# Kernel tuning notes

Measured on AMD Instinct MI355X. Metric: run time of the kernel, lower is better.

The kernel has to match this reference:

```python
import jax, jax.numpy as jnp
import numpy as np

N_NODES = 100000
N_EDGES = 1000000
F_IN = 256
HEADS = 2
C_OUT = 64
NEG_SLOPE = 0.2


def setup_inputs() -> dict:
    key = jax.random.key(0)
    k_x, k_e, k_ws, k_wd, k_a = jax.random.split(key, 5)
    x = jax.random.normal(k_x, (N_NODES, F_IN), dtype=jnp.float32)
    edge_index = jax.random.randint(k_e, (2, N_EDGES), 0, N_NODES, dtype=jnp.int64)
    # uniform init as in init_randoms('uniform'), scale is irrelevant for correctness
    W_src = jax.random.uniform(k_ws, (F_IN, HEADS * C_OUT), dtype=jnp.float32, minval=-0.1, maxval=0.1)
    W_dst = jax.random.uniform(k_wd, (F_IN, HEADS * C_OUT), dtype=jnp.float32, minval=-0.1, maxval=0.1)
    att = jax.random.uniform(k_a, (HEADS, C_OUT), dtype=jnp.float32, minval=-0.1, maxval=0.1)
    bias = jnp.zeros((HEADS * C_OUT,), dtype=jnp.float32)
    return {"x": x, "edge_index": edge_index, "W_src": W_src, "W_dst": W_dst, "att": att, "bias": bias}


def reference(x, edge_index, W_src, W_dst, att, bias):
    # GATv2 conv (MyGATConv), concat=True, add_self_loops=False, dropout=0
    N = x.shape[0]
    H, C = att.shape
    x_src = (x @ W_src).reshape(N, H, C)  # Theta_s x  [N,H,C]
    x_dst = (x @ W_dst).reshape(N, H, C)  # Theta_d x  [N,H,C]
    src = edge_index[0]  # j (source)
    dst = edge_index[1]  # i (target) -> segment index

    xj = x_src[src]                                   # [E,H,C]
    e = jax.nn.leaky_relu(xj + x_dst[dst], NEG_SLOPE)  # [E,H,C]
    logits = jnp.einsum('ehc,hc->eh', e, att)          # [E,H]

    # segment softmax over destination neighborhoods
    seg_max = jax.ops.segment_max(logits, dst, num_segments=N)  # [N,H]
    seg_max = jnp.where(jnp.isfinite(seg_max), seg_max, 0.0)
    ex = jnp.exp(logits - seg_max[dst])                # [E,H]
    denom = jax.ops.segment_sum(ex, dst, num_segments=N)  # [N,H]
    alpha = ex / (denom[dst] + 1e-16)                  # [E,H]

    # scatter-add aggregation of alpha * Theta_s x_j
    out = jax.ops.segment_sum(alpha[:, :, None] * xj, dst, num_segments=N)  # [N,H,C]
    return out.reshape(N, H * C) + bias
```

## Files before the change

kernel.cpp:

```cpp
#include <hip/hip_runtime.h>

#define F_IN 256
#define HC   128

typedef __attribute__((ext_vector_type(8))) short bf16x8;
typedef __attribute__((ext_vector_type(4))) float f32x4;
typedef __attribute__((ext_vector_type(2))) float f32x2;

__device__ __forceinline__ unsigned short f2b(float f) {
    unsigned int u = __float_as_uint(f);
    return (unsigned short)((u + 0x7FFFu + ((u >> 16) & 1u)) >> 16);
}

__device__ __forceinline__ unsigned int f2b_pk(float lo, float hi) {
    unsigned int ul = __float_as_uint(lo);
    unsigned int uh = __float_as_uint(hi);
    ul = ul + 0x7FFFu + ((ul >> 16) & 1u);
    uh = uh + 0x7FFFu + ((uh >> 16) & 1u);
    return __builtin_amdgcn_perm(uh, ul, 0x07060302);
}

#define DPP_ADD(x, ctrl) \
    x += __int_as_float(__builtin_amdgcn_update_dpp(0, __float_as_int(x), ctrl, 0xF, 0xF, true))

__device__ __forceinline__ f32x2 row_sum16_2(f32x2 v) {
    DPP_ADD(v.x, 0xB1);  DPP_ADD(v.y, 0xB1);
    DPP_ADD(v.x, 0x4E);  DPP_ADD(v.y, 0x4E);
    DPP_ADD(v.x, 0x141); DPP_ADD(v.y, 0x141);
    DPP_ADD(v.x, 0x140); DPP_ADD(v.y, 0x140);
    return v;
}

__global__ __launch_bounds__(256) void k_prep(const float* __restrict__ Ws,
                                              const float* __restrict__ Wd,
                                              unsigned short* __restrict__ PB) {
    int tid = blockIdx.x * 256 + threadIdx.x;
    int nt  = tid >> 9;
    int rem = tid & 511;
    int t   = rem >> 6;
    int l   = rem & 63;
    int m   = l & 15;
    int w   = nt >> 2;
    int g   = nt & 3;
    int pos = w * 64 + m * 4 + g;
    int kbase = 32 * t + (l >> 4) * 8;

    const float* W;
    int n;
    if (pos < 128) {
        W = Ws; n = (pos & 1) * 64 + (pos >> 1);
    } else {
        int p2 = pos - 128;
        W = Wd; n = (p2 & 1) * 64 + (p2 >> 1);
    }
    union { bf16x8 v; unsigned short u[8]; } o;
#pragma unroll
    for (int j = 0; j < 8; ++j)
        o.u[j] = f2b(W[(kbase + j) * HC + n]);
    *(bf16x8*)(PB + (size_t)tid * 8) = o.v;
}

#define LIST_BLOCKS 1024
__global__ __launch_bounds__(256) void k_gemm_list(const float* __restrict__ x,
                                                   const unsigned short* __restrict__ PB,
                                                   unsigned short* __restrict__ xsrc_pk,
                                                   unsigned short* __restrict__ xdst_pk, int N,
                                                   const int* __restrict__ src,
                                                   const int* __restrict__ dst, int E,
                                                   int* __restrict__ head1,
                                                   uint2* __restrict__ rec) {
    if (blockIdx.x < LIST_BLOCKS) {
        int i = blockIdx.x * 256 + threadIdx.x;
        int stride = LIST_BLOCKS * 256;
        for (; i < E; i += stride) {
            int d = dst[i];
            int s = src[i];
            int old = atomicExch(&head1[d], i);
            rec[i] = make_uint2((unsigned int)old, (unsigned int)s);
        }
        return;
    }

    __shared__ unsigned short smem[64 * F_IN];
    char* sb = (char*)smem;

    const int wave = threadIdx.x >> 6;
    const int lane = threadIdx.x & 63;
    const int m = lane & 15;
    const int q = lane >> 4;
    const long row0 = (long)(blockIdx.x - LIST_BLOCKS) * 64;

    {
        const int col = lane * 4;
        const int wbyte_base = col * 2;
#pragma unroll 8
        for (int i = 0; i < 16; ++i) {
            int row = i * 4 + wave;
            long grow = row0 + row;
            if (grow >= N) grow = N - 1;
            float4 a = *(const float4*)(x + grow * F_IN + col);
            uint2 v;
            v.x = f2b_pk(a.x, a.y);
            v.y = f2b_pk(a.z, a.w);
            *(uint2*)(sb + row * 512 + (wbyte_base ^ ((row & 7) << 4))) = v;
        }
    }
    __syncthreads();

    f32x4 acc[4][4];
#pragma unroll
    for (int a = 0; a < 4; ++a)
#pragma unroll
        for (int b = 0; b < 4; ++b) acc[a][b] = (f32x4){0.f, 0.f, 0.f, 0.f};

#pragma unroll
    for (int t = 0; t < 8; ++t) {
        const int bytein = t * 64 + q * 16;
        bf16x8 af[4];
#pragma unroll
        for (int mt = 0; mt < 4; ++mt) {
            const int row = mt * 16 + m;
            af[mt] = *(const bf16x8*)(sb + row * 512 + (bytein ^ ((row & 7) << 4)));
        }
#pragma unroll
        for (int g = 0; g < 4; ++g) {
            const int nt = wave * 4 + g;
            bf16x8 bf = *(const bf16x8*)(PB + ((size_t)(nt * 8 + t) * 64 + lane) * 8);
#pragma unroll
            for (int mt = 0; mt < 4; ++mt)
                acc[mt][g] = __builtin_amdgcn_mfma_f32_16x16x32_bf16(af[mt], bf, acc[mt][g], 0, 0, 0);
        }
    }

    unsigned short* dstArr = (wave < 2) ? xsrc_pk : xdst_pk;
    const int colOff = ((wave & 1) * 64) + m * 4;
#pragma unroll
    for (int mt = 0; mt < 4; ++mt) {
#pragma unroll
        for (int r = 0; r < 4; ++r) {
            long row = row0 + mt * 16 + q * 4 + r;
            if (row >= N) continue;
            uint2 v;
            v.x = f2b_pk(acc[mt][0][r], acc[mt][1][r]);
            v.y = f2b_pk(acc[mt][2][r], acc[mt][3][r]);
            *(uint2*)(dstArr + row * HC + colOff) = v;
        }
    }
}

__global__ __launch_bounds__(256) void k_agg(const unsigned int* __restrict__ xsrc_u,
                                             const unsigned int* __restrict__ xdst_u,
                                             const int* __restrict__ head1,
                                             const uint2* __restrict__ rec,
                                             const float* __restrict__ att,
                                             const float* __restrict__ bias,
                                             float* __restrict__ out, int N) {
    const int lane = threadIdx.x & 63;
    const int s = lane & 15;
    const int node = blockIdx.x * 16 + (threadIdx.x >> 4);
    const bool vn = node < N;
    const int nc = vn ? node : 0;

    uint4 D = *(const uint4*)(xdst_u + (size_t)nc * 64 + s * 4);
    f32x2 xd[4], at[4];
    {
        unsigned int du[4] = {D.x, D.y, D.z, D.w};
#pragma unroll
        for (int k = 0; k < 4; ++k)
            xd[k] = (f32x2){__uint_as_float(du[k] << 16),
                            __uint_as_float(du[k] & 0xFFFF0000u)};
    }
    {
        float4 A0 = *(const float4*)(att + s * 4);
        float4 A1 = *(const float4*)(att + 64 + s * 4);
        at[0] = (f32x2){A0.x, A1.x}; at[1] = (f32x2){A0.y, A1.y};
        at[2] = (f32x2){A0.z, A1.z}; at[3] = (f32x2){A0.w, A1.w};
    }

    f32x2 l2 = (f32x2){0.f, 0.f};
    f32x2 o2[4];
#pragma unroll
    for (int k = 0; k < 4; ++k) o2[k] = (f32x2){0.f, 0.f};

    int e = vn ? head1[nc] : -1;
    uint2 r = rec[e >= 0 ? e : 0];
    int j = (e >= 0) ? (int)r.y : 0;
    uint4 U = *(const uint4*)(xsrc_u + (size_t)j * 64 + s * 4);

    while (__any(e >= 0)) {
        if (e >= 0) {
            int en = (int)r.x;
            uint2 rn = rec[en >= 0 ? en : 0];

            unsigned int cu[4] = {U.x, U.y, U.z, U.w};
            f32x2 xj[4];
            f32x2 s2 = (f32x2){0.f, 0.f};
#pragma unroll
            for (int k = 0; k < 4; ++k) {
                xj[k] = (f32x2){__uint_as_float(cu[k] << 16),
                                __uint_as_float(cu[k] & 0xFFFF0000u)};
                f32x2 e2 = xj[k] + xd[k];
                f32x2 e5 = e2 * 0.2f;
                f32x2 le;
                le.x = fmaxf(e2.x, e5.x);
                le.y = fmaxf(e2.y, e5.y);
                s2 += at[k] * le;
            }

            int jn = (en >= 0) ? (int)rn.y : 0;
            uint4 Un = *(const uint4*)(xsrc_u + (size_t)jn * 64 + s * 4);

            s2 = row_sum16_2(s2);
            f32x2 w2;
            w2.x = __expf(s2.x);
            w2.y = __expf(s2.y);
            l2 += w2;
#pragma unroll
            for (int k = 0; k < 4; ++k) o2[k] += w2 * xj[k];

            e = en; r = rn; U = Un;
        }
    }

    if (vn) {
        float inv0 = __builtin_amdgcn_rcpf(l2.x + 1e-16f);
        float inv1 = __builtin_amdgcn_rcpf(l2.y + 1e-16f);
        float4 B0 = *(const float4*)(bias + s * 4);
        float4 B1 = *(const float4*)(bias + 64 + s * 4);
        float4 R0 = {o2[0].x * inv0 + B0.x, o2[1].x * inv0 + B0.y,
                     o2[2].x * inv0 + B0.z, o2[3].x * inv0 + B0.w};
        float4 R1 = {o2[0].y * inv1 + B1.x, o2[1].y * inv1 + B1.y,
                     o2[2].y * inv1 + B1.z, o2[3].y * inv1 + B1.w};
        *(float4*)(out + (size_t)node * HC + s * 4) = R0;
        *(float4*)(out + (size_t)node * HC + 64 + s * 4) = R1;
    }
}

extern "C" void kernel_launch(void* const* d_in, const int* in_sizes, int n_in,
                              void* d_out, int out_size, void* d_ws, size_t ws_size,
                              hipStream_t stream) {
    const float* x    = (const float*)d_in[0];
    const int*   ei   = (const int*)d_in[1];
    const float* Ws   = (const float*)d_in[2];
    const float* Wd   = (const float*)d_in[3];
    const float* att  = (const float*)d_in[4];
    const float* bias = (const float*)d_in[5];
    float* out = (float*)d_out;

    const int N = in_sizes[0] / F_IN;
    const int E = in_sizes[1] / 2;
    const int* src = ei;
    const int* dst = ei + E;

    char* ws = (char*)d_ws;
    size_t off = 0;
    auto alloc = [&](size_t bytes) -> char* {
        off = (off + 255) & ~(size_t)255;
        char* p = ws + off;
        off += bytes;
        return p;
    };
    unsigned short* xsrc_pk = (unsigned short*)alloc((size_t)N * HC * sizeof(unsigned short));
    unsigned short* xdst_pk = (unsigned short*)alloc((size_t)N * HC * sizeof(unsigned short));
    unsigned short* PB = (unsigned short*)alloc(256 * 256 * sizeof(unsigned short));
    int*   head1 = (int*)alloc((size_t)N * sizeof(int));
    uint2* rec   = (uint2*)alloc((size_t)E * sizeof(uint2));

    hipMemsetAsync(head1, 0xFF, (size_t)N * sizeof(int), stream);

    k_prep<<<32, 256, 0, stream>>>(Ws, Wd, PB);
    k_gemm_list<<<LIST_BLOCKS + (int)((N + 63) / 64), 256, 0, stream>>>(
        x, PB, xsrc_pk, xdst_pk, N, src, dst, E, head1, rec);
    k_agg<<<(N + 15) / 16, 256, 0, stream>>>((const unsigned int*)xsrc_pk,
                                             (const unsigned int*)xdst_pk,
                                             head1, rec, att, bias, out, N);
}
```

Baseline: 286.1 us.

## Use 512-thread blocks for fused GEMM/list kernel and reorder list blocks last

The combined GEMM and edge-list kernel now launches 512-thread blocks. Each GEMM block still covers 64 rows, but the work is split over 8 waves, so each wave holds a 32x64 accumulator tile instead of 64x64. This lowers per-thread register pressure and should allow more resident waves. The edge-list builder blocks move from the start of the grid to the end, which changes how the two kinds of work are scheduled against each other. In exchange, each wave reuses less of its B-fragment loads and there are more waves per block to synchronise.

```diff
diff --git a/kernel.cpp b/kernel.cpp
--- a/kernel.cpp
+++ b/kernel.cpp
@@ -60,18 +60,19 @@
     *(bf16x8*)(PB + (size_t)tid * 8) = o.v;
 }
 
-#define LIST_BLOCKS 1024
-__global__ __launch_bounds__(256) void k_gemm_list(const float* __restrict__ x,
-                                                   const unsigned short* __restrict__ PB,
-                                                   unsigned short* __restrict__ xsrc_pk,
-                                                   unsigned short* __restrict__ xdst_pk, int N,
-                                                   const int* __restrict__ src,
-                                                   const int* __restrict__ dst, int E,
-                                                   int* __restrict__ head1,
-                                                   uint2* __restrict__ rec) {
-    if (blockIdx.x < LIST_BLOCKS) {
-        int i = blockIdx.x * 256 + threadIdx.x;
-        int stride = LIST_BLOCKS * 256;
+#define LIST_BLOCKS 512
+__global__ __launch_bounds__(512, 4) void k_gemm_list(const float* __restrict__ x,
+                                                      const unsigned short* __restrict__ PB,
+                                                      unsigned short* __restrict__ xsrc_pk,
+                                                      unsigned short* __restrict__ xdst_pk, int N,
+                                                      int ngemm,
+                                                      const int* __restrict__ src,
+                                                      const int* __restrict__ dst, int E,
+                                                      int* __restrict__ head1,
+                                                      uint2* __restrict__ rec) {
+    if (blockIdx.x >= ngemm) {
+        int i = (blockIdx.x - ngemm) * 512 + threadIdx.x;
+        int stride = LIST_BLOCKS * 512;
         for (; i < E; i += stride) {
             int d = dst[i];
             int s = src[i];
@@ -88,61 +89,62 @@
     const int lane = threadIdx.x & 63;
     const int m = lane & 15;
     const int q = lane >> 4;
-    const long row0 = (long)(blockIdx.x - LIST_BLOCKS) * 64;
+    const int w4 = wave & 3;
+    const int wm = wave >> 2;
+    const long row0 = (long)blockIdx.x * 64;
 
     {
         const int col = lane * 4;
-        const int wbyte_base = col * 2;
-#pragma unroll 8
-        for (int i = 0; i < 16; ++i) {
-            int row = i * 4 + wave;
+        const int wb = col * 2;
+#pragma unroll
+        for (int i = 0; i < 8; ++i) {
+            int row = i * 8 + wave;
             long grow = row0 + row;
             if (grow >= N) grow = N - 1;
             float4 a = *(const float4*)(x + grow * F_IN + col);
             uint2 v;
             v.x = f2b_pk(a.x, a.y);
             v.y = f2b_pk(a.z, a.w);
-            *(uint2*)(sb + row * 512 + (wbyte_base ^ ((row & 7) << 4))) = v;
+            *(uint2*)(sb + row * 512 + (wb ^ ((row & 7) << 4))) = v;
         }
     }
     __syncthreads();
 
-    f32x4 acc[4][4];
-#pragma unroll
-    for (int a = 0; a < 4; ++a)
+    f32x4 acc[2][4];
+#pragma unroll
+    for (int a = 0; a < 2; ++a)
 #pragma unroll
         for (int b = 0; b < 4; ++b) acc[a][b] = (f32x4){0.f, 0.f, 0.f, 0.f};
 
 #pragma unroll
     for (int t = 0; t < 8; ++t) {
         const int bytein = t * 64 + q * 16;
-        bf16x8 af[4];
-#pragma unroll
-        for (int mt = 0; mt < 4; ++mt) {
-            const int row = mt * 16 + m;
-            af[mt] = *(const bf16x8*)(sb + row * 512 + (bytein ^ ((row & 7) << 4)));
+        bf16x8 af[2];
+#pragma unroll
+        for (int mt2 = 0; mt2 < 2; ++mt2) {
+            const int row = wm * 32 + mt2 * 16 + m;
+            af[mt2] = *(const bf16x8*)(sb + row * 512 + (bytein ^ ((row & 7) << 4)));
         }
 #pragma unroll
         for (int g = 0; g < 4; ++g) {
-            const int nt = wave * 4 + g;
+            const int nt = w4 * 4 + g;
             bf16x8 bf = *(const bf16x8*)(PB + ((size_t)(nt * 8 + t) * 64 + lane) * 8);
-#pragma unroll
-            for (int mt = 0; mt < 4; ++mt)
-                acc[mt][g] = __builtin_amdgcn_mfma_f32_16x16x32_bf16(af[mt], bf, acc[mt][g], 0, 0, 0);
-        }
-    }
-
-    unsigned short* dstArr = (wave < 2) ? xsrc_pk : xdst_pk;
-    const int colOff = ((wave & 1) * 64) + m * 4;
-#pragma unroll
-    for (int mt = 0; mt < 4; ++mt) {
+            acc[0][g] = __builtin_amdgcn_mfma_f32_16x16x32_bf16(af[0], bf, acc[0][g], 0, 0, 0);
+            acc[1][g] = __builtin_amdgcn_mfma_f32_16x16x32_bf16(af[1], bf, acc[1][g], 0, 0, 0);
+        }
+    }
+
+    unsigned short* dstArr = (w4 < 2) ? xsrc_pk : xdst_pk;
+    const int colOff = ((w4 & 1) * 64) + m * 4;
+#pragma unroll
+    for (int mt2 = 0; mt2 < 2; ++mt2) {
 #pragma unroll
         for (int r = 0; r < 4; ++r) {
-            long row = row0 + mt * 16 + q * 4 + r;
+            long row = row0 + wm * 32 + mt2 * 16 + q * 4 + r;
             if (row >= N) continue;
             uint2 v;
-            v.x = f2b_pk(acc[mt][0][r], acc[mt][1][r]);
-            v.y = f2b_pk(acc[mt][2][r], acc[mt][3][r]);
+            v.x = f2b_pk(acc[mt2][0][r], acc[mt2][1][r]);
+            v.y = f2b_pk(acc[mt2][2][r], acc[mt2][3][r]);
             *(uint2*)(dstArr + row * HC + colOff) = v;
         }
     }
@@ -268,9 +270,10 @@
 
     hipMemsetAsync(head1, 0xFF, (size_t)N * sizeof(int), stream);
 
+    const int ngemm = (N + 63) / 64;
     k_prep<<<32, 256, 0, stream>>>(Ws, Wd, PB);
-    k_gemm_list<<<LIST_BLOCKS + (int)((N + 63) / 64), 256, 0, stream>>>(
-        x, PB, xsrc_pk, xdst_pk, N, src, dst, E, head1, rec);
+    k_gemm_list<<<ngemm + LIST_BLOCKS, 512, 0, stream>>>(
+        x, PB, xsrc_pk, xdst_pk, N, ngemm, src, dst, E, head1, rec);
     k_agg<<<(N + 15) / 16, 256, 0, stream>>>((const unsigned int*)xsrc_pk,
                                              (const unsigned int*)xdst_pk,
                                              head1, rec, att, bias, out, N);
```

Result: slower. 307.2 us (+7.4%).

## Replace per-node linked edge list with bucketed neighbor slots plus overflow chain

Applied to the files above, without the earlier changes.

Edge bucketing now uses four per-node sub-counters with up to 8 slots each, storing source indices directly in a dense per-node array. Only overflow edges fall back to the atomicExch linked list. In aggregation, neighbor indices come from the dense array, so the next source row can be prefetched without first chasing a dependent rec load. This costs an extra memset, a 128-byte-per-node index array and atomicAdd contention on the counters.

```diff
diff --git a/kernel.cpp b/kernel.cpp
--- a/kernel.cpp
+++ b/kernel.cpp
@@ -67,6 +67,8 @@
                                                    unsigned short* __restrict__ xdst_pk, int N,
                                                    const int* __restrict__ src,
                                                    const int* __restrict__ dst, int E,
+                                                   int* __restrict__ cnt4,
+                                                   int* __restrict__ eidx,
                                                    int* __restrict__ head1,
                                                    uint2* __restrict__ rec) {
     if (blockIdx.x < LIST_BLOCKS) {
@@ -75,8 +77,14 @@
         for (; i < E; i += stride) {
             int d = dst[i];
             int s = src[i];
-            int old = atomicExch(&head1[d], i);
-            rec[i] = make_uint2((unsigned int)old, (unsigned int)s);
+            int sub = i & 3;
+            int slot = atomicAdd(&cnt4[(size_t)d * 4 + sub], 1);
+            if (slot < 8) {
+                eidx[(size_t)d * 32 + sub * 8 + slot] = s;
+            } else {
+                int old = atomicExch(&head1[d], i);
+                rec[i] = make_uint2((unsigned int)old, (unsigned int)s);
+            }
         }
         return;
     }
@@ -150,6 +158,8 @@
 
 __global__ __launch_bounds__(256) void k_agg(const unsigned int* __restrict__ xsrc_u,
                                              const unsigned int* __restrict__ xdst_u,
+                                             const int* __restrict__ cnt4,
+                                             const int* __restrict__ eidx,
                                              const int* __restrict__ head1,
                                              const uint2* __restrict__ rec,
                                              const float* __restrict__ att,
@@ -182,15 +192,31 @@
 #pragma unroll
     for (int k = 0; k < 4; ++k) o2[k] = (f32x2){0.f, 0.f};
 
-    int e = vn ? head1[nc] : -1;
-    uint2 r = rec[e >= 0 ? e : 0];
-    int j = (e >= 0) ? (int)r.y : 0;
+    uint4 c4 = *(const uint4*)(cnt4 + (size_t)nc * 4);
+    int d0 = min((int)c4.x, 8), d1 = min((int)c4.y, 8);
+    int d2 = min((int)c4.z, 8), d3 = min((int)c4.w, 8);
+    const int p1 = d0, p2 = d0 + d1, p3 = d0 + d1 + d2;
+    const int T  = vn ? (p3 + d3) : 0;
+    const int* nb = eidx + (size_t)nc * 32;
+
+    auto nbidx = [&](int t) -> int {
+        int pos = (t < p1) ? t
+                : (t < p2) ? (8  + t - p1)
+                : (t < p3) ? (16 + t - p2)
+                :            (24 + t - p3);
+        return nb[pos];
+    };
+
+    int t = 0;
+    bool act = t < T;
+    int j = act ? nbidx(0) : 0;
     uint4 U = *(const uint4*)(xsrc_u + (size_t)j * 64 + s * 4);
 
-    while (__any(e >= 0)) {
-        if (e >= 0) {
-            int en = (int)r.x;
-            uint2 rn = rec[en >= 0 ? en : 0];
+    while (__any(act)) {
+        if (act) {
+            bool actn = (t + 1) < T;
+            int jn = actn ? nbidx(t + 1) : 0;
+            uint4 Un = *(const uint4*)(xsrc_u + (size_t)jn * 64 + s * 4);
 
             unsigned int cu[4] = {U.x, U.y, U.z, U.w};
             f32x2 xj[4];
@@ -207,9 +233,6 @@
                 s2 += at[k] * le;
             }
 
-            int jn = (en >= 0) ? (int)rn.y : 0;
-            uint4 Un = *(const uint4*)(xsrc_u + (size_t)jn * 64 + s * 4);
-
             s2 = row_sum16_2(s2);
             f32x2 w2;
             w2.x = __expf(s2.x);
@@ -218,7 +241,42 @@
 #pragma unroll
             for (int k = 0; k < 4; ++k) o2[k] += w2 * xj[k];
 
-            e = en; r = rn; U = Un;
+            t = t + 1; act = actn; U = Un;
+        }
+    }
+
+    int e = vn ? head1[nc] : -1;
+    if (__any(e >= 0)) {
+        uint2 r = rec[e >= 0 ? e : 0];
+        while (__any(e >= 0)) {
+            if (e >= 0) {
+                int jo = (int)r.y;
+                uint4 Uo = *(const uint4*)(xsrc_u + (size_t)jo * 64 + s * 4);
+                int en = (int)r.x;
+                if (en >= 0) r = rec[en];
+                unsigned int cu[4] = {Uo.x, Uo.y, Uo.z, Uo.w};
+                f32x2 xj[4];
+                f32x2 s2 = (f32x2){0.f, 0.f};
+#pragma unroll
+                for (int k = 0; k < 4; ++k) {
+                    xj[k] = (f32x2){__uint_as_float(cu[k] << 16),
+                                    __uint_as_float(cu[k] & 0xFFFF0000u)};
+                    f32x2 e2 = xj[k] + xd[k];
+                    f32x2 e5 = e2 * 0.2f;
+                    f32x2 le;
+                    le.x = fmaxf(e2.x, e5.x);
+                    le.y = fmaxf(e2.y, e5.y);
+                    s2 += at[k] * le;
+                }
+                s2 = row_sum16_2(s2);
+                f32x2 w2;
+                w2.x = __expf(s2.x);
+                w2.y = __expf(s2.y);
+                l2 += w2;
+#pragma unroll
+                for (int k = 0; k < 4; ++k) o2[k] += w2 * xj[k];
+                e = en;
+            }
         }
     }
 
@@ -263,15 +321,18 @@
     unsigned short* xsrc_pk = (unsigned short*)alloc((size_t)N * HC * sizeof(unsigned short));
     unsigned short* xdst_pk = (unsigned short*)alloc((size_t)N * HC * sizeof(unsigned short));
     unsigned short* PB = (unsigned short*)alloc(256 * 256 * sizeof(unsigned short));
+    int*   cnt4  = (int*)alloc((size_t)N * 4 * sizeof(int));
     int*   head1 = (int*)alloc((size_t)N * sizeof(int));
+    int*   eidx  = (int*)alloc((size_t)N * 32 * sizeof(int));
     uint2* rec   = (uint2*)alloc((size_t)E * sizeof(uint2));
 
+    hipMemsetAsync(cnt4, 0, (size_t)N * 4 * sizeof(int), stream);
     hipMemsetAsync(head1, 0xFF, (size_t)N * sizeof(int), stream);
 
     k_prep<<<32, 256, 0, stream>>>(Ws, Wd, PB);
     k_gemm_list<<<LIST_BLOCKS + (int)((N + 63) / 64), 256, 0, stream>>>(
-        x, PB, xsrc_pk, xdst_pk, N, src, dst, E, head1, rec);
+        x, PB, xsrc_pk, xdst_pk, N, src, dst, E, cnt4, eidx, head1, rec);
     k_agg<<<(N + 15) / 16, 256, 0, stream>>>((const unsigned int*)xsrc_pk,
                                              (const unsigned int*)xdst_pk,
-                                             head1, rec, att, bias, out, N);
-}
+                                             cnt4, eidx, head1, rec, att, bias, out, N);
+}
```

Result: slower. 316.5 us (+10.6%).
